# Performance work log

Hardware: AMD Instinct MI355X
Metric: run time of the kernel (lower is better)

The kernel has to match this reference:

```python
import jax, jax.numpy as jnp
import numpy as np

B = 16384      # batch
N = 128        # number of DNPU nodes (experts)
I = 3          # data electrodes per node
C = 4          # control electrodes per node
E = I + C      # total electrodes = 7
H = 90         # surrogate-model hidden width
L = 3          # number of extra hidden layers


def setup_inputs() -> dict:
    key = jax.random.key(0)
    ks = jax.random.split(key, 8)
    s_in = 1.0 / np.sqrt(E)
    s_h = 1.0 / np.sqrt(H)
    return {
        "x": jax.random.normal(ks[0], (B, N * I), dtype=jnp.float32),
        "controls": jax.random.uniform(ks[1], (N, C), dtype=jnp.float32, minval=-1.2, maxval=0.6),
        "W_in": jax.random.normal(ks[2], (N, E, H), dtype=jnp.float32) * s_in,
        "b_in": jax.random.normal(ks[3], (N, H), dtype=jnp.float32) * 0.1,
        "W_hid": jax.random.normal(ks[4], (L, N, H, H), dtype=jnp.float32) * s_h,
        "b_hid": jax.random.normal(ks[5], (L, N, H), dtype=jnp.float32) * 0.1,
        "W_out": jax.random.normal(ks[6], (N, H), dtype=jnp.float32) * s_h,
        "b_out": jax.random.normal(ks[7], (N,), dtype=jnp.float32) * 0.1,
    }


def reference(x, controls, W_in, b_in, W_hid, b_hid, W_out, b_out):
    # DNPU_Layer: partition x into N chunks of I, each node merges its data
    # electrodes with its learned control voltages into a 7-electrode vector,
    # evaluates the shared surrogate MLP with per-node parameters, outputs 1
    # current per node; results are concatenated along dim 1 -> [B, N].
    b = x.shape[0]
    xd = x.reshape(b, N, I)                                   # partition_input
    ctrl = jnp.broadcast_to(controls[None], (b, N, C))        # per-node controls
    e = jnp.concatenate([xd, ctrl], axis=-1)                  # [B, N, E]
    h = jax.nn.relu(jnp.einsum('bne,neh->bnh', e, W_in) + b_in)
    for l in range(L):  # fixed small layer count
        h = jax.nn.relu(jnp.einsum('bnh,nhk->bnk', h, W_hid[l]) + b_hid[l])
    out = jnp.einsum('bnh,nh->bn', h, W_out) + b_out          # [B, N]
    return out
```

## Files before the change

kernel.cpp:

```cpp
#include <hip/hip_runtime.h>
#include <stdint.h>

namespace {
constexpr int kB  = 16384;
constexpr int kN  = 128;
constexpr int kI  = 3;
constexpr int kC  = 4;
constexpr int kH  = 90;
constexpr int kL  = 3;
constexpr int BT  = 64;
constexpr int KP  = 96;
constexpr int FB_PER_NODE = 57;
constexpr int NODE_USH    = FB_PER_NODE * 512;
constexpr size_t WT_BYTES = (size_t)kN * NODE_USH * 2;
constexpr size_t WO_OFF   = WT_BYTES;
constexpr size_t XK_OFF   = WO_OFF + (size_t)kN * KP * 4;
constexpr size_t OT_OFF   = XK_OFF + (size_t)kN * kI * kB * 2;
}

typedef __attribute__((ext_vector_type(8))) short bf16x8;
typedef __attribute__((ext_vector_type(4))) float f32x4;
typedef __attribute__((ext_vector_type(16))) float f32x16;

__device__ __forceinline__ uint32_t pack_bf16(float lo, float hi) {
#if __has_builtin(__builtin_amdgcn_cvt_pk_bf16_f32)
  auto r = __builtin_amdgcn_cvt_pk_bf16_f32(lo, hi);
  union { decltype(r) v; uint32_t u; } c; c.v = r; return c.u;
#else
  union { float f; uint32_t i; } a, b; a.f = lo; b.f = hi;
  uint32_t ua = a.i + 0x8000u;
  uint32_t ub = b.i + 0x8000u;
  return __builtin_amdgcn_perm(ub, ua, 0x07060302);
#endif
}
__device__ __forceinline__ ushort f2bf(float f) {
  union { float f; uint32_t i; } v; v.f = f;
  uint32_t u = v.i + 0x7FFFu + ((v.i >> 16) & 1u);
  return (ushort)(u >> 16);
}

__device__ __forceinline__ void pl32swap(uint32_t& a, uint32_t& b) {
#if __has_builtin(__builtin_amdgcn_permlane32_swap)
  auto r = __builtin_amdgcn_permlane32_swap(a, b, false, false);
  a = (uint32_t)r[0]; b = (uint32_t)r[1];
#else
  uint32_t sa = (uint32_t)__shfl_xor((int)a, 32);
  uint32_t sb = (uint32_t)__shfl_xor((int)b, 32);
  bool lo = (threadIdx.x & 63) < 32;
  uint32_t na = lo ? a : sb;
  uint32_t nb = lo ? sa : b;
  a = na; b = nb;
#endif
}

__global__ __launch_bounds__(256) void prep_kernel(
    const float* __restrict__ x,
    const float* __restrict__ W_in, const float* __restrict__ b_in,
    const float* __restrict__ W_hid, const float* __restrict__ b_hid,
    const float* __restrict__ W_out, const float* __restrict__ b_out,
    ushort* __restrict__ wt, float* __restrict__ wo, ushort* __restrict__ xk)
{
  __shared__ float smem[kH * (kH + 1) + kH];
  const int tid = threadIdx.x;
  const int bid = blockIdx.x;

  if (bid < 4 * kN) {
    float* ldsw = smem;
    float* ldsb = smem + kH * (kH + 1);
    const int node  = bid & (kN - 1);
    const int layer = bid >> 7;
    const int ksrc  = (layer == 0) ? (kI + kC) : kH;
    const float* src;
    const float* bsrc;
    if (layer == 0) { src = W_in + (size_t)node * (kI + kC) * kH; bsrc = b_in + (size_t)node * kH; }
    else {
      int l = layer - 1;
      src  = W_hid + (size_t)(l * kN + node) * kH * kH;
      bsrc = b_hid + (size_t)(l * kN + node) * kH;
    }
    for (int idx = tid; idx < ksrc * kH; idx += 256)
      ldsw[(idx / kH) * (kH + 1) + (idx % kH)] = src[idx];
    if (tid < kH) ldsb[tid] = bsrc[tid];
    __syncthreads();
    ushort* dstbase = wt + (size_t)node * NODE_USH
                    + (size_t)((layer == 0) ? 0 : 3 + (layer - 1) * 18) * 512;
    const int nch = (layer == 0) ? 192 : 1152;
#pragma unroll
    for (int it = 0; it < 5; ++it) {
      int c = tid + it * 256;
      if (c < nch) {
        int fb = c >> 6, lane = c & 63;
        int ks = (layer == 0) ? 0 : fb / 3;
        int mt = (layer == 0) ? fb : fb % 3;
        int j  = mt * 32 + (lane & 31);
        int kb = ks * 16 + (lane >> 5) * 8;
        float v[8];
#pragma unroll
        for (int i = 0; i < 8; ++i) {
          int k = kb + i;
          float t = 0.f;
          if (j < kH) {
            if (k < ksrc)       t = ldsw[k * (kH + 1) + j];
            else if (k == ksrc) t = ldsb[j];
          }
          v[i] = t;
        }
        uint4 p;
        p.x = pack_bf16(v[0], v[1]); p.y = pack_bf16(v[2], v[3]);
        p.z = pack_bf16(v[4], v[5]); p.w = pack_bf16(v[6], v[7]);
        *(uint4*)&dstbase[(size_t)c * 8] = p;
      }
    }
  } else if (bid < 4 * kN + 4) {
    int base = (bid - 4 * kN) * 3072;
    for (int t = 0; t < 12; ++t) {
      int idx = base + t * 256 + tid;
      int node = idx / KP, j = idx % KP;
      float v = 0.f;
      if (j < kH)       v = W_out[node * kH + j];
      else if (j == kH) v = b_out[node];
      wo[idx] = v;
    }
  } else {
    int xb = bid - (4 * kN + 4);
    int b0 = (xb & 255) * 64;
    int c0 = (xb >> 8) * 96;
    float* lds = smem;
    for (int idx = tid; idx < 64 * 96; idx += 256) {
      int r = idx / 96, c = idx % 96;
      lds[r * 97 + c] = x[(size_t)(b0 + r) * (kN * kI) + c0 + c];
    }
    __syncthreads();
#pragma unroll
    for (int it = 0; it < 3; ++it) {
      int c = tid + it * 256;
      int nk = c >> 3, b = (c & 7) * 8;
      float v[8];
#pragma unroll
      for (int i = 0; i < 8; ++i) v[i] = lds[(b + i) * 97 + nk];
      uint4 p;
      p.x = pack_bf16(v[0], v[1]); p.y = pack_bf16(v[2], v[3]);
      p.z = pack_bf16(v[4], v[5]); p.w = pack_bf16(v[6], v[7]);
      *(uint4*)&xk[(size_t)(c0 + nk) * kB + b0 + b] = p;
    }
  }
}

__global__ __launch_bounds__(64, 3) void dnpu_kernel(
    const ushort* __restrict__ xk, const float* __restrict__ controls,
    const ushort* __restrict__ wt, const float* __restrict__ wo,
    float* __restrict__ outT)
{
  const int lane = threadIdx.x;
  const int node = (int)(blockIdx.x & 127);
  const int m0   = (int)(blockIdx.x >> 7) * BT;
  const int col  = lane & 31;
  const int hh   = lane >> 5;

  const f32x16 zf = (f32x16)0.0f;
  f32x16 acc[3][2];

  bf16x8 b0[2];
  {
    const ushort cb0 = f2bf(controls[node * kC + 0]);
    const ushort cb1 = f2bf(controls[node * kC + 1]);
    const ushort cb2 = f2bf(controls[node * kC + 2]);
    const ushort cb3 = f2bf(controls[node * kC + 3]);
    const ushort* xp = xk + (size_t)node * kI * kB + m0 + col;
#pragma unroll
    for (int nt = 0; nt < 2; ++nt) {
      union { ushort s[8]; bf16x8 v; } f;
      f.s[0] = xp[0 * kB + nt * 32];
      f.s[1] = xp[1 * kB + nt * 32];
      f.s[2] = xp[2 * kB + nt * 32];
      f.s[3] = cb0; f.s[4] = cb1; f.s[5] = cb2; f.s[6] = cb3;
      f.s[7] = 0x3F80;
      bf16x8 z = (bf16x8){0,0,0,0,0,0,0,0};
      if (hh) b0[nt] = z; else b0[nt] = f.v;
    }
  }

  {
    const ushort* t0 = wt + (size_t)node * NODE_USH;
#pragma unroll
    for (int mt = 0; mt < 3; ++mt) {
      bf16x8 afr = *(const bf16x8*)&t0[mt * 512 + lane * 8];
#pragma unroll
      for (int nt = 0; nt < 2; ++nt)
        acc[mt][nt] = __builtin_amdgcn_mfma_f32_32x32x16_bf16(afr, b0[nt], zf, 0, 0, 0);
    }
  }

  union BF { uint32_t u[4]; bf16x8 v; };
  BF Bw[6][2];

  auto packB = [&]() {
#pragma unroll
    for (int mt = 0; mt < 3; ++mt)
#pragma unroll
      for (int nt = 0; nt < 2; ++nt) {
        float v[16];
#pragma unroll
        for (int r = 0; r < 16; ++r) v[r] = fmaxf(acc[mt][nt][r], 0.f);
        if (mt == 2) v[14] = (hh == 0) ? 1.0f : v[14];
        uint32_t P[8];
#pragma unroll
        for (int w = 0; w < 8; ++w) P[w] = pack_bf16(v[2 * w], v[2 * w + 1]);
        uint32_t a0 = P[0], c0 = P[2]; pl32swap(a0, c0);
        uint32_t a1 = P[1], c1 = P[3]; pl32swap(a1, c1);
        uint32_t a2 = P[4], c2 = P[6]; pl32swap(a2, c2);
        uint32_t a3 = P[5], c3 = P[7]; pl32swap(a3, c3);
        Bw[2 * mt][nt].u[0] = a0; Bw[2 * mt][nt].u[1] = a1;
        Bw[2 * mt][nt].u[2] = c0; Bw[2 * mt][nt].u[3] = c1;
        Bw[2 * mt + 1][nt].u[0] = a2; Bw[2 * mt + 1][nt].u[1] = a3;
        Bw[2 * mt + 1][nt].u[2] = c2; Bw[2 * mt + 1][nt].u[3] = c3;
      }
  };

#pragma unroll
  for (int l = 0; l < kL; ++l) {
    packB();
    const ushort* tl = wt + (size_t)node * NODE_USH + (size_t)(3 + l * 18) * 512;
#pragma unroll
    for (int ks = 0; ks < 6; ++ks)
#pragma unroll
      for (int mt = 0; mt < 3; ++mt) {
        bf16x8 afr = *(const bf16x8*)&tl[(size_t)(ks * 3 + mt) * 512 + lane * 8];
#pragma unroll
        for (int nt = 0; nt < 2; ++nt)
          acc[mt][nt] = __builtin_amdgcn_mfma_f32_32x32x16_bf16(
              afr, Bw[ks][nt].v, (ks == 0) ? zf : acc[mt][nt], 0, 0, 0);
      }
  }

  {
    const float* wop = wo + node * KP;
    float s0 = 0.f, s1 = 0.f;
#pragma unroll
    for (int mt = 0; mt < 3; ++mt) {
#pragma unroll
      for (int g = 0; g < 4; ++g) {
        float4 wf = *(const float4*)&wop[mt * 32 + g * 8 + hh * 4];
#pragma unroll
        for (int r2 = 0; r2 < 4; ++r2) {
          int r = g * 4 + r2;
          float w = (r2 == 0) ? wf.x : (r2 == 1) ? wf.y : (r2 == 2) ? wf.z : wf.w;
          float h0v = fmaxf(acc[mt][0][r], 0.f);
          float h1v = fmaxf(acc[mt][1][r], 0.f);
          if (mt == 2 && r == 14) {
            h0v = (hh == 0) ? 1.0f : h0v;
            h1v = (hh == 0) ? 1.0f : h1v;
          }
          s0 += h0v * w; s1 += h1v * w;
        }
      }
    }
    s0 += __shfl_xor(s0, 32);
    s1 += __shfl_xor(s1, 32);
    float r = hh ? s1 : s0;
    outT[(size_t)node * kB + m0 + lane] = r;
  }
}

__global__ __launch_bounds__(256) void transpose_out(
    const float* __restrict__ ot, float* __restrict__ out)
{
  __shared__ float t[64][65];
  const int b0 = (int)(blockIdx.x & 255) * 64;
  const int n0 = (int)(blockIdx.x >> 8) * 64;
  const int c  = threadIdx.x & 63;
  const int r4 = threadIdx.x >> 6;
#pragma unroll
  for (int i = 0; i < 16; ++i) {
    int n = r4 + i * 4;
    t[n][c] = ot[(size_t)(n0 + n) * kB + b0 + c];
  }
  __syncthreads();
#pragma unroll
  for (int i = 0; i < 16; ++i) {
    int b = r4 + i * 4;
    out[(size_t)(b0 + b) * kN + n0 + c] = t[c][b];
  }
}

extern "C" void kernel_launch(void* const* d_in, const int* in_sizes, int n_in,
                              void* d_out, int out_size, void* d_ws, size_t ws_size,
                              hipStream_t stream) {
  const float* x        = (const float*)d_in[0];
  const float* controls = (const float*)d_in[1];
  const float* W_in     = (const float*)d_in[2];
  const float* b_in     = (const float*)d_in[3];
  const float* W_hid    = (const float*)d_in[4];
  const float* b_hid    = (const float*)d_in[5];
  const float* W_out    = (const float*)d_in[6];
  const float* b_out    = (const float*)d_in[7];
  float* out = (float*)d_out;

  ushort* wt = (ushort*)d_ws;
  float*  wo = (float*)((char*)d_ws + WO_OFF);
  ushort* xk = (ushort*)((char*)d_ws + XK_OFF);
  float*  ot = (float*)((char*)d_ws + OT_OFF);

  hipLaunchKernelGGL(prep_kernel, dim3(4 * kN + 4 + 1024), dim3(256), 0, stream,
                     x, W_in, b_in, W_hid, b_hid, W_out, b_out, wt, wo, xk);

  dim3 grid((kB / BT) * kN);
  hipLaunchKernelGGL(dnpu_kernel, grid, dim3(64), 0, stream,
                     xk, controls, wt, wo, ot);

  hipLaunchKernelGGL(transpose_out, dim3(512), dim3(256), 0, stream, ot, out);
}
```

Before: 244.3 us.

## Share per-node weights across four waves via double-buffered LDS async staging

Each block now holds four waves that process 256 batch rows of the same node instead of one wave per 64 rows. Per-layer hidden weights are loaded once per block into LDS with global_load_lds and double-buffered, so the next layer's load overlaps the current layer's MFMAs. Matrix work is wrapped in s_setprio. This cuts redundant global and L2 weight reads by a factor of four. It adds block-level barriers, about 36KB of LDS per block that may limit occupancy, and a smaller grid.

```diff
diff --git a/kernel.cpp b/kernel.cpp
--- a/kernel.cpp
+++ b/kernel.cpp
@@ -8,7 +8,6 @@
 constexpr int kC  = 4;
 constexpr int kH  = 90;
 constexpr int kL  = 3;
-constexpr int BT  = 64;
 constexpr int KP  = 96;
 constexpr int FB_PER_NODE = 57;
 constexpr int NODE_USH    = FB_PER_NODE * 512;
@@ -51,6 +50,12 @@
   uint32_t nb = lo ? sa : b;
   a = na; b = nb;
 #endif
+}
+
+__device__ __forceinline__ void stage16(const ushort* g, ushort* l) {
+  __builtin_amdgcn_global_load_lds(
+      (const __attribute__((address_space(1))) void*)g,
+      (__attribute__((address_space(3))) void*)l, 16, 0, 0);
 }
 
 __global__ __launch_bounds__(256) void prep_kernel(
@@ -146,16 +151,37 @@
   }
 }
 
-__global__ __launch_bounds__(64, 3) void dnpu_kernel(
+__global__ __launch_bounds__(256, 3) void dnpu_kernel(
     const ushort* __restrict__ xk, const float* __restrict__ controls,
     const ushort* __restrict__ wt, const float* __restrict__ wo,
     float* __restrict__ outT)
 {
-  const int lane = threadIdx.x;
+  __shared__ __align__(16) ushort wbuf[2][18 * 512];
+
+  const int tid  = threadIdx.x;
+  const int lane = tid & 63;
+  const int wid  = tid >> 6;
   const int node = (int)(blockIdx.x & 127);
-  const int m0   = (int)(blockIdx.x >> 7) * BT;
+  const int m0   = (int)(blockIdx.x >> 7) * 256 + wid * 64;
   const int col  = lane & 31;
   const int hh   = lane >> 5;
+
+  const ushort* wnode = wt + (size_t)node * NODE_USH;
+
+  auto stage_hid = [&](int l, ushort* buf) {
+    const ushort* src = wnode + (size_t)(3 + l * 18) * 512;
+#pragma unroll
+    for (int r = 0; r < 4; ++r)
+      stage16(src + (size_t)(r * 256 + wid * 64 + lane) * 8,
+              buf + (size_t)(r * 256 + wid * 64) * 8);
+    if (wid < 2)
+      stage16(src + (size_t)(1024 + wid * 64 + lane) * 8,
+              buf + (size_t)(1024 + wid * 64) * 8);
+  };
+
+  if (wid < 3)
+    stage16(wnode + (size_t)(wid * 64 + lane) * 8, &wbuf[0][(size_t)(wid * 64) * 8]);
+  stage_hid(0, &wbuf[1][0]);
 
   const f32x16 zf = (f32x16)0.0f;
   f32x16 acc[3][2];
@@ -177,17 +203,6 @@
       f.s[7] = 0x3F80;
       bf16x8 z = (bf16x8){0,0,0,0,0,0,0,0};
       if (hh) b0[nt] = z; else b0[nt] = f.v;
-    }
-  }
-
-  {
-    const ushort* t0 = wt + (size_t)node * NODE_USH;
-#pragma unroll
-    for (int mt = 0; mt < 3; ++mt) {
-      bf16x8 afr = *(const bf16x8*)&t0[mt * 512 + lane * 8];
-#pragma unroll
-      for (int nt = 0; nt < 2; ++nt)
-        acc[mt][nt] = __builtin_amdgcn_mfma_f32_32x32x16_bf16(afr, b0[nt], zf, 0, 0, 0);
     }
   }
 
@@ -217,21 +232,48 @@
       }
   };
 
-#pragma unroll
-  for (int l = 0; l < kL; ++l) {
-    packB();
-    const ushort* tl = wt + (size_t)node * NODE_USH + (size_t)(3 + l * 18) * 512;
+  auto compute_hidden = [&](const ushort* buf) {
+    __builtin_amdgcn_s_setprio(1);
 #pragma unroll
     for (int ks = 0; ks < 6; ++ks)
 #pragma unroll
       for (int mt = 0; mt < 3; ++mt) {
-        bf16x8 afr = *(const bf16x8*)&tl[(size_t)(ks * 3 + mt) * 512 + lane * 8];
+        bf16x8 afr = *(const bf16x8*)&buf[(size_t)(ks * 3 + mt) * 512 + lane * 8];
 #pragma unroll
         for (int nt = 0; nt < 2; ++nt)
           acc[mt][nt] = __builtin_amdgcn_mfma_f32_32x32x16_bf16(
               afr, Bw[ks][nt].v, (ks == 0) ? zf : acc[mt][nt], 0, 0, 0);
       }
-  }
+    __builtin_amdgcn_s_setprio(0);
+  };
+
+  __syncthreads();
+
+  {
+    __builtin_amdgcn_s_setprio(1);
+#pragma unroll
+    for (int mt = 0; mt < 3; ++mt) {
+      bf16x8 afr = *(const bf16x8*)&wbuf[0][(size_t)mt * 512 + lane * 8];
+#pragma unroll
+      for (int nt = 0; nt < 2; ++nt)
+        acc[mt][nt] = __builtin_amdgcn_mfma_f32_32x32x16_bf16(afr, b0[nt], zf, 0, 0, 0);
+    }
+    __builtin_amdgcn_s_setprio(0);
+  }
+
+  packB();
+  __syncthreads();
+  stage_hid(1, &wbuf[0][0]);
+  compute_hidden(&wbuf[1][0]);
+
+  packB();
+  __syncthreads();
+  stage_hid(2, &wbuf[1][0]);
+  compute_hidden(&wbuf[0][0]);
+
+  packB();
+  __syncthreads();
+  compute_hidden(&wbuf[1][0]);
 
   {
     const float* wop = wo + node * KP;
@@ -304,8 +346,8 @@
   hipLaunchKernelGGL(prep_kernel, dim3(4 * kN + 4 + 1024), dim3(256), 0, stream,
                      x, W_in, b_in, W_hid, b_hid, W_out, b_out, wt, wo, xk);
 
-  dim3 grid((kB / BT) * kN);
-  hipLaunchKernelGGL(dnpu_kernel, grid, dim3(64), 0, stream,
+  dim3 grid((kB / 256) * kN);
+  hipLaunchKernelGGL(dnpu_kernel, grid, dim3(256), 0, stream,
                      xk, controls, wt, wo, ot);
 
   hipLaunchKernelGGL(transpose_out, dim3(512), dim3(256), 0, stream, ot, out);
```

Result: faster. 219.7 us (-10.1%).
